# Optimization experiments

Hardware: AMD Instinct MI355X
Metric: run time of the kernel (lower is better)

Reference implementation:

```python
import jax, jax.numpy as jnp
import numpy as np

N = 100_000      # nodes
E = 1_600_000    # edges (avg degree 16)
D_IN = 64        # input feature size
H = 4            # num_heads
F = 16           # out_feats per head
EFST = 1e-3      # norm clamp from source


def setup_inputs() -> dict:
    key = jax.random.key(0)
    k0, k1, k2, k3, k4, k5 = jax.random.split(key, 6)
    feat = jax.random.normal(k0, (N, D_IN), dtype=jnp.float32)
    src = jax.random.randint(k1, (E,), 0, N, dtype=jnp.int32)
    dst = jax.random.randint(k2, (E,), 0, N, dtype=jnp.int32)
    W = jax.random.normal(k3, (H * F, D_IN), dtype=jnp.float32) * 0.1   # fc.weight
    attn_l = jax.random.normal(k4, (H, F), dtype=jnp.float32) * 0.1
    attn_r = jax.random.normal(k5, (H, F), dtype=jnp.float32) * 0.1
    return dict(feat=feat, src=src, dst=dst, W=W, attn_l=attn_l, attn_r=attn_r)


def reference(feat, src, dst, W, attn_l, attn_r):
    n = feat.shape[0]
    h, f = attn_l.shape
    # fc projection -> (N, H, F)
    z = (feat @ W.T).reshape(n, h, f)
    # attention logits per node per head
    el = jnp.einsum('nhf,hf->nh', z, attn_l)  # (N, H)
    er = jnp.einsum('nhf,hf->nh', z, attn_r)  # (N, H)
    # per-node squared-feature sums over heads, clamped (source: ft[ft<efst]=efst)
    s = jnp.maximum(jnp.sum(z * z, axis=1), EFST)  # (N, F)
    inv_s = 1.0 / s
    # edge-level gathers
    zu = z[src]                                   # (E, H, F)
    zv = z[dst]                                   # (E, H, F)
    edp = jnp.einsum('ehf,ehf->eh', zu, zv)       # u_dot_v(ft, ftd)
    edp_ftfd = jnp.einsum('ef,ef->e', inv_s[src], inv_s[dst])  # per-edge scalar
    e_sum = el[src] + er[dst]                     # u_add_v(el, er) -> (E, H)
    escore = jax.nn.relu(edp * edp_ftfd[:, None]) * e_sum       # (E, H)
    # edge_softmax over incoming edges per dst node, per head
    m = jax.ops.segment_max(escore, dst, num_segments=n)        # (N, H)
    m = jnp.where(jnp.isfinite(m), m, 0.0)                      # empty segments
    ex = jnp.exp(escore - m[dst])                               # (E, H)
    denom = jax.ops.segment_sum(ex, dst, num_segments=n)        # (N, H)
    a = ex / jnp.where(denom[dst] > 0, denom[dst], 1.0)         # (E, H)
    # aggregate: u_mul_e(ft, a) then sum per dst
    out = jax.ops.segment_sum(a[:, :, None] * zu, dst, num_segments=n)  # (N, H, F)
    return out
```

## Files before the change

### kernel.cpp

```cpp
#include <hip/hip_runtime.h>
#include <hip/hip_fp16.h>
#include <math.h>

#define DIN 64
#define LOG2E 1.44269504f
#define DEFER_THR 11.5415603f
#define BKT_CAP 5120
#define EPB 4096
#define SRC_MASK 0x1FFFFF


__device__ __forceinline__ float fast_exp2(float x) {
    float r; asm("v_exp_f32 %0, %1" : "=v"(r) : "v"(x)); return r;
}
__device__ __forceinline__ int rfl(int x) { return __builtin_amdgcn_readfirstlane(x); }

typedef _Float16 half2_t __attribute__((ext_vector_type(2)));
typedef _Float16 f16x8 __attribute__((ext_vector_type(8)));
typedef float f32x4 __attribute__((ext_vector_type(4)));

__device__ __forceinline__ float fdot2(float a_raw, float b_raw, float acc) {
    half2_t a = __builtin_bit_cast(half2_t, a_raw);
    half2_t b = __builtin_bit_cast(half2_t, b_raw);
    return __builtin_amdgcn_fdot2(a, b, acc, false);
}

__device__ __forceinline__ void split8(const float* p, f16x8& hi, f16x8& lo) {
    float4 v0 = *(const float4*)p;
    float4 v1 = *(const float4*)(p + 4);
    float vv[8] = {v0.x, v0.y, v0.z, v0.w, v1.x, v1.y, v1.z, v1.w};
#pragma unroll
    for (int i = 0; i < 8; i++) {
        _Float16 h = (_Float16)vv[i];
        hi[i] = h;
        lo[i] = (_Float16)(vv[i] - (float)h);
    }
}

template<int CTRL>
__device__ __forceinline__ float dppmov(float x) {
    union { float f; int i; } u, r;
    u.f = x;
    r.i = __builtin_amdgcn_update_dpp(0, u.i, CTRL, 0xF, 0xF, true);
    return r.f;
}
__device__ __forceinline__ float rowsum16(float x) {
    x += dppmov<0xB1>(x);
    x += dppmov<0x4E>(x);
    x += dppmov<0x124>(x);
    x += dppmov<0x128>(x);
    return x;
}
__device__ __forceinline__ float rowsum8(float x) {
    x += dppmov<0xB1>(x);
    x += dppmov<0x4E>(x);
    x += dppmov<0x141>(x);
    return x;
}

__global__ __launch_bounds__(256) void build_all(
    const float* __restrict__ feat, const float* __restrict__ W,
    const float* __restrict__ attn_l, const float* __restrict__ attn_r,
    const int* __restrict__ src, const int* __restrict__ dst, int e_n,
    int* __restrict__ gcur, unsigned int* __restrict__ pairs,
    __half* __restrict__ zrec, float* __restrict__ misc, int n, int nbkt)
{
    int bid = blockIdx.x;
    if ((bid & 1) == 0) {
        int base = (bid >> 1) * EPB;
        int tid = threadIdx.x;
        int wv = tid >> 6;
        __shared__ int hist4[4][400];
        __shared__ int curb[400];
        for (int i = tid; i < 4 * 400; i += 256) ((int*)hist4)[i] = 0;
        __syncthreads();
        int d[16], s[16];
#pragma unroll
        for (int k = 0; k < 16; k++) {
            int idx = base + k * 256 + tid;
            bool val = idx < e_n;
            d[k] = val ? dst[idx] : -1;
            s[k] = val ? src[idx] : 0;
            if (val) atomicAdd(&hist4[wv][d[k] >> 8], 1);
        }
        __syncthreads();
        for (int i = tid; i < nbkt; i += 256) {
            int c = hist4[0][i] + hist4[1][i] + hist4[2][i] + hist4[3][i];
            curb[i] = (c > 0) ? atomicAdd(&gcur[i], c) : 0;
        }
        __syncthreads();
#pragma unroll
        for (int k = 0; k < 16; k++) {
            if (d[k] >= 0) {
                int b = d[k] >> 8;
                int pos = atomicAdd(&curb[b], 1);
                if (pos < BKT_CAP)
                    pairs[(size_t)b * BKT_CAP + pos] =
                        (unsigned int)s[k] | ((unsigned int)(d[k] & 255) << 21);
            }
        }
        return;
    }
    int mb = bid >> 1;

    int lane = threadIdx.x & 63;
    int col = lane & 15;
    int kg  = lane >> 4;

    f16x8 bhi[4][2], blo[4][2];
#pragma unroll
    for (int t = 0; t < 4; t++) {
#pragma unroll
        for (int kh = 0; kh < 2; kh++) {
            const float* wp = W + (size_t)(16 * t + col) * 64 + kh * 32 + kg * 8;
            split8(wp, bhi[t][kh], blo[t][kh]);
        }
    }

    float al[4], ar[4];
#pragma unroll
    for (int t = 0; t < 4; t++) {
        al[t] = attn_l[t * 16 + col];
        ar[t] = attn_r[t * 16 + col];
    }

    int wti = mb * 4 + (threadIdx.x >> 6);

#pragma unroll 1
    for (int it = 0; it < 4; it++) {
        int nb = (wti * 4 + it) * 16;
        if (nb >= n) break;
        int arow = nb + col; if (arow > n - 1) arow = n - 1;
        const float* ap = feat + (size_t)arow * 64 + kg * 8;
        f16x8 ahi0, alo0, ahi1, alo1;
        split8(ap, ahi0, alo0);
        split8(ap + 32, ahi1, alo1);

        f32x4 c[4];
#pragma unroll
        for (int t = 0; t < 4; t++) {
            f32x4 acc = {0.f, 0.f, 0.f, 0.f};
            acc = __builtin_amdgcn_mfma_f32_16x16x32_f16(alo0, bhi[t][0], acc, 0, 0, 0);
            acc = __builtin_amdgcn_mfma_f32_16x16x32_f16(ahi0, blo[t][0], acc, 0, 0, 0);
            acc = __builtin_amdgcn_mfma_f32_16x16x32_f16(ahi0, bhi[t][0], acc, 0, 0, 0);
            acc = __builtin_amdgcn_mfma_f32_16x16x32_f16(alo1, bhi[t][1], acc, 0, 0, 0);
            acc = __builtin_amdgcn_mfma_f32_16x16x32_f16(ahi1, blo[t][1], acc, 0, 0, 0);
            acc = __builtin_amdgcn_mfma_f32_16x16x32_f16(ahi1, bhi[t][1], acc, 0, 0, 0);
            c[t] = acc;
        }

#pragma unroll
        for (int j = 0; j < 4; j++) {
            int rr = nb + kg * 4 + j;
            if (rr >= n) continue;
            float z0 = c[0][j], z1 = c[1][j], z2 = c[2][j], z3 = c[3][j];

            float sq = z0 * z0 + z1 * z1 + z2 * z2 + z3 * z3;
            float isv = 1.0f / fmaxf(sq, 1e-3f);

            float e0 = rowsum16(z0 * al[0]) * LOG2E;
            float e1 = rowsum16(z1 * al[1]) * LOG2E;
            float e2 = rowsum16(z2 * al[2]) * LOG2E;
            float e3 = rowsum16(z3 * al[3]) * LOG2E;
            float r0 = rowsum16(z0 * ar[0]) * LOG2E;
            float r1 = rowsum16(z1 * ar[1]) * LOG2E;
            float r2 = rowsum16(z2 * ar[2]) * LOG2E;
            float r3 = rowsum16(z3 * ar[3]) * LOG2E;

            __half* zp = zrec + (size_t)rr * 64;
            zp[col]      = __float2half_rn(z0);
            zp[16 + col] = __float2half_rn(z1);
            zp[32 + col] = __float2half_rn(z2);
            zp[48 + col] = __float2half_rn(z3);

            float* mf = misc + (size_t)rr * 16;
            ((__half*)mf)[col] = __float2half_rn(isv);
            if (col == 0) {
                mf[8]  = e0; mf[9]  = e1; mf[10] = e2; mf[11] = e3;
                mf[12] = r0; mf[13] = r1; mf[14] = r2; mf[15] = r3;
            }
        }
    }
}

__global__ __launch_bounds__(256) void bucket_csr(
    const unsigned int* __restrict__ pairs, const int* __restrict__ gcur,
    int* __restrict__ perm, int2* __restrict__ srow, int n)
{
    int b = blockIdx.x;
    int tid = threadIdx.x;
    int count = min(gcur[b], BKT_CAP);

    __shared__ unsigned int plds[BKT_CAP];
    __shared__ int hist[256], sums[256], cur2[256];

    for (int i = tid; i < count; i += 256) plds[i] = pairs[(size_t)b * BKT_CAP + i];
    hist[tid] = 0;
    __syncthreads();
    for (int i = tid; i < count; i += 256) atomicAdd(&hist[plds[i] >> 21], 1);
    __syncthreads();
    int hv = hist[tid];
    sums[tid] = hv;
    __syncthreads();
    for (int off = 1; off < 256; off <<= 1) {
        int x = (tid >= off) ? sums[tid - off] : 0;
        __syncthreads();
        sums[tid] += x;
        __syncthreads();
    }
    int excl = sums[tid] - hv;
    int v = b * 256 + tid;
    if (v < n) srow[v] = make_int2(b * BKT_CAP + excl, hv);
    cur2[tid] = excl;
    __syncthreads();
    for (int i = tid; i < count; i += 256) {
        unsigned int p = plds[i];
        int pos = atomicAdd(&cur2[p >> 21], 1);
        perm[(size_t)b * BKT_CAP + pos] = (int)(p & SRC_MASK);
    }
}

__global__ __launch_bounds__(256) void node_fused(
    const __half* __restrict__ zrec, const float* __restrict__ misc,
    const int* __restrict__ perm, const int2* __restrict__ srow,
    float* __restrict__ out, int n)
{
    int lane = threadIdx.x & 63;
    int slot = lane >> 3;
    int l8   = lane & 7;
    int h    = l8 >> 1;
    int v = blockIdx.x * 4 + (threadIdx.x >> 6);
    if (v >= n) return;
    v = rfl(v);

    int2 sr = srow[v];
    int start = rfl(sr.x), len = rfl(sr.y);

    float* op = out + (size_t)v * 64 + 8 * l8;
    if (len == 0) {
        if (slot == 0) {
            *(float4*)op = make_float4(0.f, 0.f, 0.f, 0.f);
            *(float4*)(op + 4) = make_float4(0.f, 0.f, 0.f, 0.f);
        }
        return;
    }

    float4 zvr = *(const float4*)(zrec + (size_t)v * 64 + 8 * l8);
    const float* mv = misc + (size_t)v * 16;
    float ivr = mv[l8];
    float erv = mv[12 + h];

    int idx = start + slot;
    float w = (slot < len) ? 1.f : 0.f;
    int u = (slot < len) ? perm[idx] : v;

    float m = -INFINITY, denom = 0.f;
    float4 accA = make_float4(0.f, 0.f, 0.f, 0.f);
    float4 accB = make_float4(0.f, 0.f, 0.f, 0.f);
    int lmax = (len + 7) >> 3;

    for (int it = 0; it < lmax; ++it) {
        int rn = len - (8 * (it + 1) + slot);
        int un = (rn > 0) ? perm[idx + 8] : v;
        float wn = (rn > 0) ? 1.f : 0.f;

        float4 zur = *(const float4*)(zrec + (size_t)u * 64 + 8 * l8);
        const float* mu = misc + (size_t)u * 16;
        float iur = mu[l8];
        float eu = mu[8 + h];

        float edp = fdot2(zur.x, zvr.x,
                    fdot2(zur.y, zvr.y,
                    fdot2(zur.z, zvr.z,
                    fdot2(zur.w, zvr.w, 0.f))));
        edp += dppmov<0xB1>(edp);
        float ffp = rowsum8(fdot2(iur, ivr, 0.f));
        float s = fmaxf(edp * ffp, 0.f) * (eu + erv) * w;

        if (s > m + DEFER_THR) {
            float c = fast_exp2(m - s);
            denom *= c;
            accA.x *= c; accA.y *= c; accA.z *= c; accA.w *= c;
            accB.x *= c; accB.y *= c; accB.z *= c; accB.w *= c;
            m = s;
        }
        float p = fast_exp2(s - m) * w;
        denom += p;
        float2 z0 = __half22float2(*(__half2*)&zur.x);
        float2 z1 = __half22float2(*(__half2*)&zur.y);
        float2 z2 = __half22float2(*(__half2*)&zur.z);
        float2 z3 = __half22float2(*(__half2*)&zur.w);
        accA.x = fmaf(p, z0.x, accA.x); accA.y = fmaf(p, z0.y, accA.y);
        accA.z = fmaf(p, z1.x, accA.z); accA.w = fmaf(p, z1.y, accA.w);
        accB.x = fmaf(p, z2.x, accB.x); accB.y = fmaf(p, z2.y, accB.y);
        accB.z = fmaf(p, z3.x, accB.z); accB.w = fmaf(p, z3.y, accB.w);

        u = un; w = wn; idx += 8;
    }

    {
        float om = dppmov<0x128>(m);
        float od = dppmov<0x128>(denom);
        float oA0 = dppmov<0x128>(accA.x), oA1 = dppmov<0x128>(accA.y);
        float oA2 = dppmov<0x128>(accA.z), oA3 = dppmov<0x128>(accA.w);
        float oB0 = dppmov<0x128>(accB.x), oB1 = dppmov<0x128>(accB.y);
        float oB2 = dppmov<0x128>(accB.z), oB3 = dppmov<0x128>(accB.w);
        float mm = fmaxf(m, om);
        float cs = fast_exp2(m - mm), co = fast_exp2(om - mm);
        denom = denom * cs + od * co;
        accA.x = accA.x * cs + oA0 * co; accA.y = accA.y * cs + oA1 * co;
        accA.z = accA.z * cs + oA2 * co; accA.w = accA.w * cs + oA3 * co;
        accB.x = accB.x * cs + oB0 * co; accB.y = accB.y * cs + oB1 * co;
        accB.z = accB.z * cs + oB2 * co; accB.w = accB.w * cs + oB3 * co;
        m = mm;
    }
#pragma unroll
    for (int off = 16; off <= 32; off <<= 1) {
        float om = __shfl_xor(m, off);
        float od = __shfl_xor(denom, off);
        float oA0 = __shfl_xor(accA.x, off), oA1 = __shfl_xor(accA.y, off);
        float oA2 = __shfl_xor(accA.z, off), oA3 = __shfl_xor(accA.w, off);
        float oB0 = __shfl_xor(accB.x, off), oB1 = __shfl_xor(accB.y, off);
        float oB2 = __shfl_xor(accB.z, off), oB3 = __shfl_xor(accB.w, off);
        float mm = fmaxf(m, om);
        float cs = fast_exp2(m - mm), co = fast_exp2(om - mm);
        denom = denom * cs + od * co;
        accA.x = accA.x * cs + oA0 * co; accA.y = accA.y * cs + oA1 * co;
        accA.z = accA.z * cs + oA2 * co; accA.w = accA.w * cs + oA3 * co;
        accB.x = accB.x * cs + oB0 * co; accB.y = accB.y * cs + oB1 * co;
        accB.z = accB.z * cs + oB2 * co; accB.w = accB.w * cs + oB3 * co;
        m = mm;
    }

    if (slot == 0) {
        float inv = 1.0f / denom;
        *(float4*)op = make_float4(accA.x * inv, accA.y * inv, accA.z * inv, accA.w * inv);
        *(float4*)(op + 4) = make_float4(accB.x * inv, accB.y * inv, accB.z * inv, accB.w * inv);
    }
}

extern "C" void kernel_launch(void* const* d_in, const int* in_sizes, int n_in,
                              void* d_out, int out_size, void* d_ws, size_t ws_size,
                              hipStream_t stream)
{
    const float* feat   = (const float*)d_in[0];
    const int*   src    = (const int*)d_in[1];
    const int*   dst    = (const int*)d_in[2];
    const float* W      = (const float*)d_in[3];
    const float* attn_l = (const float*)d_in[4];
    const float* attn_r = (const float*)d_in[5];
    float* out = (float*)d_out;

    const int n   = in_sizes[0] / DIN;
    const int e_n = in_sizes[1];
    const int nbkt = (n + 255) / 256;

    __half*       zrec  = (__half*)d_ws;
    float*        misc  = (float*)(zrec + (size_t)n * 64);
    unsigned int* pairs = (unsigned int*)(misc + (size_t)n * 16);
    int*          perm  = (int*)(pairs + (size_t)nbkt * BKT_CAP);
    int2*         srow  = (int2*)(perm + (size_t)nbkt * BKT_CAP);
    int*          gcur  = (int*)(srow + n);

    hipMemsetAsync(gcur, 0, (size_t)nbkt * sizeof(int), stream);

    int mmb = (n + 255) / 256;
    hipLaunchKernelGGL(build_all, dim3(mmb * 2), dim3(256), 0, stream,
                       feat, W, attn_l, attn_r, src, dst, e_n, gcur, pairs, zrec, misc, n, nbkt);

    hipLaunchKernelGGL(bucket_csr, dim3(nbkt), dim3(256), 0, stream,
                       pairs, gcur, perm, srow, n);

    hipLaunchKernelGGL(node_fused, dim3((n + 3) / 4), dim3(256), 0, stream,
                       zrec, misc, perm, srow, out, n);
}
```

Measured before the change: 114.6 us.

## Split edge loop into full and masked tail, per-wave bucket cursors

```diff
diff --git a/kernel.cpp b/kernel.cpp
--- a/kernel.cpp
+++ b/kernel.cpp
@@ -71,7 +71,7 @@
         int tid = threadIdx.x;
         int wv = tid >> 6;
         __shared__ int hist4[4][400];
-        __shared__ int curb[400];
+        __shared__ int curb4[4][400];
         for (int i = tid; i < 4 * 400; i += 256) ((int*)hist4)[i] = 0;
         __syncthreads();
         int d[16], s[16];
@@ -85,15 +85,20 @@
         }
         __syncthreads();
         for (int i = tid; i < nbkt; i += 256) {
-            int c = hist4[0][i] + hist4[1][i] + hist4[2][i] + hist4[3][i];
-            curb[i] = (c > 0) ? atomicAdd(&gcur[i], c) : 0;
+            int c0 = hist4[0][i], c1 = hist4[1][i], c2 = hist4[2][i], c3 = hist4[3][i];
+            int tot = c0 + c1 + c2 + c3;
+            int b0 = (tot > 0) ? atomicAdd(&gcur[i], tot) : 0;
+            curb4[0][i] = b0;
+            curb4[1][i] = b0 + c0;
+            curb4[2][i] = b0 + c0 + c1;
+            curb4[3][i] = b0 + c0 + c1 + c2;
         }
         __syncthreads();
 #pragma unroll
         for (int k = 0; k < 16; k++) {
             if (d[k] >= 0) {
                 int b = d[k] >> 8;
-                int pos = atomicAdd(&curb[b], 1);
+                int pos = atomicAdd(&curb4[wv][b], 1);
                 if (pos < BKT_CAP)
                     pairs[(size_t)b * BKT_CAP + pos] =
                         (unsigned int)s[k] | ((unsigned int)(d[k] & 255) << 21);
@@ -250,22 +255,59 @@
     float ivr = mv[l8];
     float erv = mv[12 + h];
 
+    int lenFull = len >> 3;
+    int tailLen = len & 7;
     int idx = start + slot;
-    float w = (slot < len) ? 1.f : 0.f;
-    int u = (slot < len) ? perm[idx] : v;
+    int u = perm[idx];
 
     float m = -INFINITY, denom = 0.f;
     float4 accA = make_float4(0.f, 0.f, 0.f, 0.f);
     float4 accB = make_float4(0.f, 0.f, 0.f, 0.f);
-    int lmax = (len + 7) >> 3;
-
-    for (int it = 0; it < lmax; ++it) {
-        int rn = len - (8 * (it + 1) + slot);
-        int un = (rn > 0) ? perm[idx + 8] : v;
-        float wn = (rn > 0) ? 1.f : 0.f;
+
+    for (int it = 0; it < lenFull; ++it) {
+        int unext = perm[idx + 8];
 
         float4 zur = *(const float4*)(zrec + (size_t)u * 64 + 8 * l8);
         const float* mu = misc + (size_t)u * 16;
+        float iur = mu[l8];
+        float eu = mu[8 + h];
+
+        float edp = fdot2(zur.x, zvr.x,
+                    fdot2(zur.y, zvr.y,
+                    fdot2(zur.z, zvr.z,
+                    fdot2(zur.w, zvr.w, 0.f))));
+        edp += dppmov<0xB1>(edp);
+        float ffp = rowsum8(fdot2(iur, ivr, 0.f));
+        float s = fmaxf(edp * ffp, 0.f) * (eu + erv);
+
+        if (s > m + DEFER_THR) {
+            float c = fast_exp2(m - s);
+            denom *= c;
+            accA.x *= c; accA.y *= c; accA.z *= c; accA.w *= c;
+            accB.x *= c; accB.y *= c; accB.z *= c; accB.w *= c;
+            m = s;
+        }
+        float p = fast_exp2(s - m);
+        denom += p;
+        float2 z0 = __half22float2(*(__half2*)&zur.x);
+        float2 z1 = __half22float2(*(__half2*)&zur.y);
+        float2 z2 = __half22float2(*(__half2*)&zur.z);
+        float2 z3 = __half22float2(*(__half2*)&zur.w);
+        accA.x = fmaf(p, z0.x, accA.x); accA.y = fmaf(p, z0.y, accA.y);
+        accA.z = fmaf(p, z1.x, accA.z); accA.w = fmaf(p, z1.y, accA.w);
+        accB.x = fmaf(p, z2.x, accB.x); accB.y = fmaf(p, z2.y, accB.y);
+        accB.z = fmaf(p, z3.x, accB.z); accB.w = fmaf(p, z3.y, accB.w);
+
+        u = unext; idx += 8;
+    }
+
+    if (tailLen) {
+        bool valid = slot < tailLen;
+        int ut = valid ? u : v;
+        float w = valid ? 1.f : 0.f;
+
+        float4 zur = *(const float4*)(zrec + (size_t)ut * 64 + 8 * l8);
+        const float* mu = misc + (size_t)ut * 16;
         float iur = mu[l8];
         float eu = mu[8 + h];
 
@@ -294,8 +336,6 @@
         accA.z = fmaf(p, z1.x, accA.z); accA.w = fmaf(p, z1.y, accA.w);
         accB.x = fmaf(p, z2.x, accB.x); accB.y = fmaf(p, z2.y, accB.y);
         accB.z = fmaf(p, z3.x, accB.z); accB.w = fmaf(p, z3.y, accB.w);
-
-        u = un; w = wn; idx += 8;
     }
 
     {
@@ -359,7 +399,7 @@
     float*        misc  = (float*)(zrec + (size_t)n * 64);
     unsigned int* pairs = (unsigned int*)(misc + (size_t)n * 16);
     int*          perm  = (int*)(pairs + (size_t)nbkt * BKT_CAP);
-    int2*         srow  = (int2*)(perm + (size_t)nbkt * BKT_CAP);
+    int2*         srow  = (int2*)(perm + (size_t)nbkt * BKT_CAP + 64);
     int*          gcur  = (int*)(srow + n);
 
     hipMemsetAsync(gcur, 0, (size_t)nbkt * sizeof(int), stream);
```

New measurement: 113.0 us. No clear change (-1.4%).
